# Optimization experiments

Hardware: AMD Instinct MI355X
Metric: run time of the kernel (lower is better)

Reference implementation:

```python
import jax, jax.numpy as jnp
import numpy as np

B, S, D, H = 4, 2048, 1024, 16
DH = D // H

def setup_inputs() -> dict:
    key = jax.random.key(0)
    ks = jax.random.split(key, 4)
    scale = 1.0 / np.sqrt(D)
    x = jax.random.normal(ks[0], (B, S, D), dtype=jnp.float32)
    Wq = jax.random.normal(ks[1], (D, D), dtype=jnp.float32) * scale
    Wk = jax.random.normal(ks[2], (D, D), dtype=jnp.float32) * scale
    Wv = jax.random.normal(ks[3], (D, D), dtype=jnp.float32) * scale
    bq = jnp.zeros((D,), dtype=jnp.float32)
    bk = jnp.zeros((D,), dtype=jnp.float32)
    bv = jnp.zeros((D,), dtype=jnp.float32)
    # causal mask, broadcastable to [B, H, S, S]; mask==0 positions get -inf
    mask = jnp.tril(jnp.ones((S, S), dtype=bool))[None, None, :, :]
    return {"x": x, "mask": mask, "Wq": Wq, "bq": bq, "Wk": Wk, "bk": bk, "Wv": Wv, "bv": bv}

def reference(x, mask, Wq, bq, Wk, bk, Wv, bv):
    b, s, d = x.shape
    def proj(W, bias):
        # nn.Linear: x @ W.T + b, then split heads -> [b, H, s, DH]
        y = jnp.einsum('bsd,ed->bse', x, W) + bias
        return y.reshape(b, s, H, DH).transpose(0, 2, 1, 3)
    q = proj(Wq, bq)
    k = proj(Wk, bk)
    v = proj(Wv, bv)
    scores = jnp.einsum('bhqd,bhkd->bhqk', q, k) / jnp.sqrt(jnp.float32(DH))
    scores = jnp.where(mask, scores, -jnp.inf)
    attn = jax.nn.softmax(scores, axis=-1)
    out = jnp.einsum('bhqk,bhkd->bhqd', attn, v)
    return out.transpose(0, 2, 1, 3).reshape(b, s, d)
```

## Files before the change

kernel.cpp:

```cpp
#include <hip/hip_runtime.h>
#include <hip/hip_bf16.h>
#include <stdint.h>

typedef unsigned short u16;
typedef unsigned int   u32;
typedef short bf16x8 __attribute__((ext_vector_type(8)));
typedef float f32x4  __attribute__((ext_vector_type(4)));

typedef bf16x8 __attribute__((__may_alias__)) bf16x8_a;
typedef uint4  __attribute__((__may_alias__)) uint4_a;
typedef uint2  __attribute__((__may_alias__)) uint2_a;
typedef float4 __attribute__((__may_alias__)) float4_a;

#define MFMA_BF16(a,b,c) __builtin_amdgcn_mfma_f32_16x16x32_bf16((a),(b),(c),0,0,0)
#define L2E 1.44269504088896340736f

#define SEQ 2048
#define DMODEL 1024
#define NH 16
#define DH 64

__device__ __forceinline__ u32 pack_bf2(float a, float b) {
  union { __hip_bfloat162 h; u32 u; } c;
  c.h = __float22bfloat162_rn(make_float2(a, b));
  return c.u;
}

__device__ __forceinline__ u16 f2bf(float f) {
  u32 u = __builtin_bit_cast(u32, f);
  u += 0x7FFFu + ((u >> 16) & 1u);
  return (u16)(u >> 16);
}

__device__ __forceinline__ void gl_lds16(const u16* g, u16* l) {
  __builtin_amdgcn_global_load_lds(
      (const __attribute__((address_space(1))) void*)g,
      (__attribute__((address_space(3))) void*)l, 16, 0, 0);
}

__global__ __launch_bounds__(256) void cvt_all_bf16(
    const float* __restrict__ x,
    const float* __restrict__ wq, const float* __restrict__ wk, const float* __restrict__ wv,
    u16* __restrict__ xb, u16* __restrict__ oq, u16* __restrict__ ok, u16* __restrict__ ov)
{
  const int c = blockIdx.x * 256 + threadIdx.x;
  const float* s; u16* d; int off;
  if (c < (1 << 20)) { s = x; d = xb; off = c; }
  else {
    const int c2 = c - (1 << 20);
    const int w = c2 >> 17;
    off = c2 & ((1 << 17) - 1);
    s = (w == 0) ? wq : (w == 1) ? wk : wv;
    d = (w == 0) ? oq : (w == 1) ? ok : ov;
  }
  const float4_a* p = (const float4_a*)(s + (size_t)off * 8);
  float4 a = p[0], b = p[1];
  uint4 o;
  o.x = pack_bf2(a.x, a.y); o.y = pack_bf2(a.z, a.w);
  o.z = pack_bf2(b.x, b.y); o.w = pack_bf2(b.z, b.w);
  *(uint4_a*)(d + (size_t)off * 8) = o;
}

__global__ __launch_bounds__(256, 3) void qkv_gemm_bf(
    const u16* __restrict__ Xb,
    const u16* __restrict__ Wqb, const u16* __restrict__ Wkb, const u16* __restrict__ Wvb,
    const float* __restrict__ Bq, const float* __restrict__ Bk, const float* __restrict__ Bv,
    u16* __restrict__ Qo, u16* __restrict__ Ko, u16* __restrict__ Vo)
{
  __shared__ u16 As[2][128 * 32];
  __shared__ u16 Bs[2][128 * 32];

  const int tid  = threadIdx.x;
  const int lane = tid & 63;
  const int wid  = tid >> 6;
  const int l16  = lane & 15;
  const int quad = lane >> 4;
  const int wm   = (wid >> 1) * 64;
  const int wn   = (wid & 1) * 64;

  const int m0 = blockIdx.x * 128;
  const int pj = blockIdx.z;

  const u16*   Wb   = (pj == 0) ? Wqb : (pj == 1) ? Wkb : Wvb;
  const float* Bias = (pj == 0) ? Bq : (pj == 1) ? Bk : Bv;
  u16*         Out  = (pj == 0) ? Qo : (pj == 1) ? Ko : Vo;
  const float scale = (pj == 0) ? 0.125f : 1.0f;

  const int lr = lane >> 2;
  const int lc = (lane & 3) * 8;

  const u16* Arow = Xb + (size_t)m0 * DMODEL;
  const int NT = DMODEL / 32;

  for (int nsub = 0; nsub < 2; ++nsub) {
    const int n0 = blockIdx.y * 256 + nsub * 128;
    const u16* Brow = Wb + (size_t)n0 * DMODEL;

    f32x4 acc[4][4];
#pragma unroll
    for (int i = 0; i < 4; i++)
#pragma unroll
      for (int j = 0; j < 4; j++) acc[i][j] = (f32x4){0.f, 0.f, 0.f, 0.f};

#pragma unroll
    for (int c = 0; c < 2; c++) {
      const int band = c * 64 + wid * 16;
      gl_lds16(Arow + (size_t)(band + lr) * DMODEL + 0 + lc, &As[0][band * 32]);
      gl_lds16(Brow + (size_t)(band + lr) * DMODEL + 0 + lc, &Bs[0][band * 32]);
    }
#pragma unroll
    for (int c = 0; c < 2; c++) {
      const int band = c * 64 + wid * 16;
      gl_lds16(Arow + (size_t)(band + lr) * DMODEL + 32 + lc, &As[1][band * 32]);
      gl_lds16(Brow + (size_t)(band + lr) * DMODEL + 32 + lc, &Bs[1][band * 32]);
    }

    for (int t = 0; t < NT; ++t) {
      const int cur = t & 1;
      if (t < NT - 1) asm volatile("s_waitcnt vmcnt(4)" ::: "memory");
      else            asm volatile("s_waitcnt vmcnt(0)" ::: "memory");
      __builtin_amdgcn_s_barrier();

      bf16x8 a[4], b[4];
#pragma unroll
      for (int mt = 0; mt < 4; mt++)
        a[mt] = *(const bf16x8_a*)&As[cur][(wm + mt * 16 + l16) * 32 + quad * 8];
#pragma unroll
      for (int nt = 0; nt < 4; nt++)
        b[nt] = *(const bf16x8_a*)&Bs[cur][(wn + nt * 16 + l16) * 32 + quad * 8];

      asm volatile("s_waitcnt lgkmcnt(0)" ::: "memory");
      __builtin_amdgcn_sched_barrier(0);
      __builtin_amdgcn_s_barrier();

      if (t + 2 < NT) {
        const int kt2 = (t + 2) * 32;
#pragma unroll
        for (int c = 0; c < 2; c++) {
          const int band = c * 64 + wid * 16;
          gl_lds16(Arow + (size_t)(band + lr) * DMODEL + kt2 + lc, &As[cur][band * 32]);
          gl_lds16(Brow + (size_t)(band + lr) * DMODEL + kt2 + lc, &Bs[cur][band * 32]);
        }
      }

#pragma unroll
      for (int mt = 0; mt < 4; mt++)
#pragma unroll
        for (int nt = 0; nt < 4; nt++)
          acc[mt][nt] = MFMA_BF16(a[mt], b[nt], acc[mt][nt]);
    }

    if (pj == 2) {
#pragma unroll
      for (int mt = 0; mt < 4; mt++) {
#pragma unroll
        for (int nt = 0; nt < 4; nt++) {
          const int n = n0 + wn + nt * 16 + l16;
          const float bias = Bias[n];
          const int h = n >> 6, dh = n & 63;
          const int m = m0 + wm + mt * 16 + quad * 4;
          const int bb = m >> 11, ss = m & 2047;
          uint2 pk;
          pk.x = pack_bf2(acc[mt][nt][0] + bias, acc[mt][nt][1] + bias);
          pk.y = pack_bf2(acc[mt][nt][2] + bias, acc[mt][nt][3] + bias);
          *(uint2_a*)&Out[((size_t)(bb * NH + h) * DH + dh) * SEQ + ss] = pk;
        }
      }
    } else {
#pragma unroll
      for (int mt = 0; mt < 4; mt++) {
#pragma unroll
        for (int nt = 0; nt < 4; nt++) {
          const int n = n0 + wn + nt * 16 + l16;
          const float bias = Bias[n];
          const int h = n >> 6, dh = n & 63;
#pragma unroll
          for (int r = 0; r < 4; r++) {
            const int m = m0 + wm + mt * 16 + quad * 4 + r;
            const int bb = m >> 11, ss = m & 2047;
            Out[((((size_t)bb * NH + h) * SEQ + ss) << 6) + dh] = f2bf((acc[mt][nt][r] + bias) * scale);
          }
        }
      }
    }

    if (nsub == 0) {
      asm volatile("s_waitcnt vmcnt(0)" ::: "memory");
    }
  }
}

__global__ __launch_bounds__(256, 2) void qkv_gemm(
    const float* __restrict__ X,
    const float* __restrict__ Wq, const float* __restrict__ Wk, const float* __restrict__ Wv,
    const float* __restrict__ Bq, const float* __restrict__ Bk, const float* __restrict__ Bv,
    u16* __restrict__ Qo, u16* __restrict__ Ko, u16* __restrict__ Vo)
{
  __shared__ u16 As[128 * 32];
  __shared__ u16 Bs[128 * 32];

  const int tid  = threadIdx.x;
  const int lane = tid & 63;
  const int wid  = tid >> 6;
  const int l16  = lane & 15;
  const int quad = lane >> 4;
  const int wm   = (wid >> 1) * 64;
  const int wn   = (wid & 1) * 64;

  const int m0 = blockIdx.x * 128;
  const int n0 = blockIdx.y * 128;
  const int pj = blockIdx.z;

  const float* W    = (pj == 0) ? Wq : (pj == 1) ? Wk : Wv;
  const float* Bias = (pj == 0) ? Bq : (pj == 1) ? Bk : Bv;
  u16*         Out  = (pj == 0) ? Qo : (pj == 1) ? Ko : Vo;
  const float scale = (pj == 0) ? 0.125f : 1.0f;

  f32x4 acc[4][4];
#pragma unroll
  for (int i = 0; i < 4; i++)
#pragma unroll
    for (int j = 0; j < 4; j++) acc[i][j] = (f32x4){0.f, 0.f, 0.f, 0.f};

  float4 gX[4], gW[4];
#pragma unroll
  for (int i = 0; i < 4; i++) {
    const int ch = i * 256 + tid;
    const int r = ch >> 3, c = ch & 7;
    gX[i] = *(const float4_a*)(X + (size_t)(m0 + r) * DMODEL + c * 4);
    gW[i] = *(const float4_a*)(W + (size_t)(n0 + r) * DMODEL + c * 4);
  }

  for (int kt = 0; kt < DMODEL; kt += 32) {
    __syncthreads();
#pragma unroll
    for (int i = 0; i < 4; i++) {
      const int ch = i * 256 + tid;
      const int r = ch >> 3, c = ch & 7;
      uint2 xp, wp;
      xp.x = pack_bf2(gX[i].x, gX[i].y);  xp.y = pack_bf2(gX[i].z, gX[i].w);
      wp.x = pack_bf2(gW[i].x, gW[i].y);  wp.y = pack_bf2(gW[i].z, gW[i].w);
      *(uint2_a*)&As[r * 32 + c * 4] = xp;
      *(uint2_a*)&Bs[r * 32 + c * 4] = wp;
    }
    __syncthreads();

    if (kt + 32 < DMODEL) {
#pragma unroll
      for (int i = 0; i < 4; i++) {
        const int ch = i * 256 + tid;
        const int r = ch >> 3, c = ch & 7;
        gX[i] = *(const float4_a*)(X + (size_t)(m0 + r) * DMODEL + kt + 32 + c * 4);
        gW[i] = *(const float4_a*)(W + (size_t)(n0 + r) * DMODEL + kt + 32 + c * 4);
      }
    }

    bf16x8 a[4], b[4];
#pragma unroll
    for (int mt = 0; mt < 4; mt++)
      a[mt] = *(const bf16x8_a*)&As[(wm + mt * 16 + l16) * 32 + quad * 8];
#pragma unroll
    for (int nt = 0; nt < 4; nt++)
      b[nt] = *(const bf16x8_a*)&Bs[(wn + nt * 16 + l16) * 32 + quad * 8];
#pragma unroll
    for (int mt = 0; mt < 4; mt++)
#pragma unroll
      for (int nt = 0; nt < 4; nt++)
        acc[mt][nt] = MFMA_BF16(a[mt], b[nt], acc[mt][nt]);
  }

  if (pj == 2) {
#pragma unroll
    for (int mt = 0; mt < 4; mt++) {
#pragma unroll
      for (int nt = 0; nt < 4; nt++) {
        const int n = n0 + wn + nt * 16 + l16;
        const float bias = Bias[n];
        const int h = n >> 6, dh = n & 63;
        const int m = m0 + wm + mt * 16 + quad * 4;
        const int bb = m >> 11, ss = m & 2047;
        uint2 pk;
        pk.x = pack_bf2(acc[mt][nt][0] + bias, acc[mt][nt][1] + bias);
        pk.y = pack_bf2(acc[mt][nt][2] + bias, acc[mt][nt][3] + bias);
        *(uint2_a*)&Out[((size_t)(bb * NH + h) * DH + dh) * SEQ + ss] = pk;
      }
    }
  } else {
#pragma unroll
    for (int mt = 0; mt < 4; mt++) {
#pragma unroll
      for (int nt = 0; nt < 4; nt++) {
        const int n = n0 + wn + nt * 16 + l16;
        const float bias = Bias[n];
        const int h = n >> 6, dh = n & 63;
#pragma unroll
        for (int r = 0; r < 4; r++) {
          const int m = m0 + wm + mt * 16 + quad * 4 + r;
          const int bb = m >> 11, ss = m & 2047;
          Out[((((size_t)bb * NH + h) * SEQ + ss) << 6) + dh] = f2bf((acc[mt][nt][r] + bias) * scale);
        }
      }
    }
  }
}

__global__ __launch_bounds__(256, 3) void flash_attn(
    const u16* __restrict__ Q, const u16* __restrict__ K, const u16* __restrict__ VT,
    float* __restrict__ O)
{
  __shared__ u16 Ks[2][64 * 64];
  __shared__ u16 VTs[2][64 * 64];
  __shared__ u16 Ps[4 * 32 * 72];

  const int tid  = threadIdx.x;
  const int lane = tid & 63;
  const int wid  = tid >> 6;
  const int l16  = lane & 15;
  const int quad = lane >> 4;

  const int idx = blockIdx.x;
  const int qt  = 15 - (idx >> 6);
  const int bh  = idx & 63;
  const int bb = bh >> 4, hh = bh & 15;
  const int qbase = qt * 128;

  const u16* Qh = Q  + (size_t)bh * (SEQ * DH);
  const u16* Kh = K  + (size_t)bh * (SEQ * DH);
  const u16* Vh = VT + (size_t)bh * (DH * SEQ);

#pragma unroll
  for (int i = 0; i < 4; i++) {
    const int ch = i * 256 + tid;
    const int r = ch >> 3, c = ch & 7;
    *(uint4_a*)&Ps[r * 72 + c * 8] = *(const uint4_a*)(Qh + (size_t)(qbase + r) * DH + c * 8);
  }
  __syncthreads();

  u16* Pw = &Ps[wid * 32 * 72];
  bf16x8 qf[2][2];
#pragma unroll
  for (int ct = 0; ct < 2; ct++)
#pragma unroll
    for (int ks = 0; ks < 2; ks++)
      qf[ct][ks] = *(const bf16x8_a*)&Pw[(ct * 16 + l16) * 72 + ks * 32 + quad * 8];

  bf16x8 ones;
#pragma unroll
  for (int i = 0; i < 8; i++) ones[i] = (short)0x3F80;

  f32x4 o[4][2];
#pragma unroll
  for (int dt = 0; dt < 4; dt++)
#pragma unroll
    for (int ct = 0; ct < 2; ct++) o[dt][ct] = (f32x4){0.f, 0.f, 0.f, 0.f};

  f32x4 lacc[2] = {(f32x4){0.f,0.f,0.f,0.f}, (f32x4){0.f,0.f,0.f,0.f}};
  float mold[2] = {-1e30f, -1e30f};

  const int jmax = 2 * qt + 1;
  const int swz  = (l16 & 7) << 3;

  uint4 gK[2], gV[2];
#pragma unroll
  for (int i = 0; i < 2; i++) {
    const int ch = i * 256 + tid;
    gK[i] = *(const uint4_a*)(Kh + (size_t)(ch >> 3) * DH + (ch & 7) * 8);
    gV[i] = *(const uint4_a*)(Vh + (size_t)(ch >> 3) * SEQ + (ch & 7) * 8);
  }
  asm volatile("s_waitcnt vmcnt(0)" ::: "memory");
#pragma unroll
  for (int i = 0; i < 2; i++) {
    const int ch = i * 256 + tid;
    const int row = ch >> 3, col = (ch & 7) * 8;
    *(uint4_a*)&Ks[0][row * 64 + (col ^ ((row & 7) << 3))]  = gK[i];
    *(uint4_a*)&VTs[0][row * 64 + (col ^ ((row & 7) << 3))] = gV[i];
  }
#pragma unroll
  for (int i = 0; i < 2; i++) {
    const int ch = i * 256 + tid;
    gK[i] = *(const uint4_a*)(Kh + (size_t)(64 + (ch >> 3)) * DH + (ch & 7) * 8);
    gV[i] = *(const uint4_a*)(Vh + (size_t)(ch >> 3) * SEQ + 64 + (ch & 7) * 8);
  }
  asm volatile("s_waitcnt lgkmcnt(0)" ::: "memory");
  __builtin_amdgcn_sched_barrier(0);
  __builtin_amdgcn_s_barrier();

  for (int j = 0; j <= jmax; j++) {
    const int cur = j & 1;
    const u16* Kc = Ks[cur];
    const u16* Vc = VTs[cur];

    f32x4 s[4][2];
#pragma unroll
    for (int rt = 0; rt < 4; rt++) {
      bf16x8 ka0 = *(const bf16x8_a*)&Kc[(rt * 16 + l16) * 64 + ((0  + quad * 8) ^ swz)];
      bf16x8 ka1 = *(const bf16x8_a*)&Kc[(rt * 16 + l16) * 64 + ((32 + quad * 8) ^ swz)];
#pragma unroll
      for (int ct = 0; ct < 2; ct++) {
        f32x4 c = (f32x4){0.f, 0.f, 0.f, 0.f};
        c = MFMA_BF16(ka0, qf[ct][0], c);
        c = MFMA_BF16(ka1, qf[ct][1], c);
        s[rt][ct] = c;
      }
    }

    if (j >= (qt << 1)) {
      const int kvb = j * 64;
#pragma unroll
      for (int rt = 0; rt < 4; rt++)
#pragma unroll
        for (int ct = 0; ct < 2; ct++) {
          const int ql = qbase + wid * 32 + ct * 16 + l16;
#pragma unroll
          for (int r = 0; r < 4; r++) {
            const int kvg = kvb + rt * 16 + quad * 4 + r;
            if (kvg > ql) s[rt][ct][r] = -1e30f;
          }
        }
    }

    if (j < jmax) {
      asm volatile("s_waitcnt vmcnt(0)" ::: "memory");
      const int nxt = cur ^ 1;
#pragma unroll
      for (int i = 0; i < 2; i++) {
        const int ch = i * 256 + tid;
        const int row = ch >> 3, col = (ch & 7) * 8;
        *(uint4_a*)&Ks[nxt][row * 64 + (col ^ ((row & 7) << 3))]  = gK[i];
        *(uint4_a*)&VTs[nxt][row * 64 + (col ^ ((row & 7) << 3))] = gV[i];
      }
      if (j + 1 < jmax) {
        const int kb2 = (j + 2) * 64;
#pragma unroll
        for (int i = 0; i < 2; i++) {
          const int ch = i * 256 + tid;
          gK[i] = *(const uint4_a*)(Kh + (size_t)(kb2 + (ch >> 3)) * DH + (ch & 7) * 8);
          gV[i] = *(const uint4_a*)(Vh + (size_t)(ch >> 3) * SEQ + kb2 + (ch & 7) * 8);
        }
      }
    }

#pragma unroll
    for (int ct = 0; ct < 2; ct++) {
      float m0_ = fmaxf(fmaxf(s[0][ct][0], s[0][ct][1]), fmaxf(s[0][ct][2], s[0][ct][3]));
      float m1_ = fmaxf(fmaxf(s[1][ct][0], s[1][ct][1]), fmaxf(s[1][ct][2], s[1][ct][3]));
      float m2_ = fmaxf(fmaxf(s[2][ct][0], s[2][ct][1]), fmaxf(s[2][ct][2], s[2][ct][3]));
      float m3_ = fmaxf(fmaxf(s[3][ct][0], s[3][ct][1]), fmaxf(s[3][ct][2], s[3][ct][3]));
      const float mloc = fmaxf(fmaxf(m0_, m1_), fmaxf(m2_, m3_));

      if (!__all(mloc - mold[ct] <= 8.0f)) {
        float mt = fmaxf(mloc, __shfl_xor(mloc, 16));
        mt = fmaxf(mt, __shfl_xor(mt, 32));
        const float mnew = fmaxf(mold[ct], mt);
        const float a = __builtin_amdgcn_exp2f((mold[ct] - mnew) * L2E);
        mold[ct] = mnew;
#pragma unroll
        for (int dt = 0; dt < 4; dt++)
#pragma unroll
          for (int r = 0; r < 4; r++) o[dt][ct][r] *= a;
#pragma unroll
        for (int r = 0; r < 4; r++) lacc[ct][r] *= a;
      }
      const float mref = mold[ct];

#pragma unroll
      for (int rt = 0; rt < 4; rt++)
#pragma unroll
        for (int r = 0; r < 4; r++)
          s[rt][ct][r] = __builtin_amdgcn_exp2f((s[rt][ct][r] - mref) * L2E);
    }

#pragma unroll
    for (int rt = 0; rt < 4; rt++) {
#pragma unroll
      for (int ct = 0; ct < 2; ct++) {
        uint2 pk;
        pk.x = pack_bf2(s[rt][ct][0], s[rt][ct][1]);
        pk.y = pack_bf2(s[rt][ct][2], s[rt][ct][3]);
        *(uint2_a*)&Pw[(ct * 16 + l16) * 72 + rt * 16 + quad * 4] = pk;
      }
    }
    asm volatile("s_waitcnt lgkmcnt(0)" ::: "memory");
    __builtin_amdgcn_sched_barrier(0);

#pragma unroll
    for (int ks2 = 0; ks2 < 2; ks2++) {
      bf16x8 vt[4], pb[2];
#pragma unroll
      for (int dt = 0; dt < 4; dt++)
        vt[dt] = *(const bf16x8_a*)&Vc[(dt * 16 + l16) * 64 + ((ks2 * 32 + quad * 8) ^ swz)];
#pragma unroll
      for (int ct = 0; ct < 2; ct++)
        pb[ct] = *(const bf16x8_a*)&Pw[(ct * 16 + l16) * 72 + ks2 * 32 + quad * 8];
#pragma unroll
      for (int dt = 0; dt < 4; dt++)
#pragma unroll
        for (int ct = 0; ct < 2; ct++)
          o[dt][ct] = MFMA_BF16(vt[dt], pb[ct], o[dt][ct]);
#pragma unroll
      for (int ct = 0; ct < 2; ct++)
        lacc[ct] = MFMA_BF16(ones, pb[ct], lacc[ct]);
    }

    __builtin_amdgcn_sched_barrier(0);
    __builtin_amdgcn_s_barrier();
  }

#pragma unroll
  for (int ct = 0; ct < 2; ct++) {
    const float inv = 1.0f / lacc[ct][0];
    const int qg = qbase + wid * 32 + ct * 16 + l16;
    float* orow = O + (size_t)((size_t)bb * SEQ + qg) * DMODEL + hh * 64;
#pragma unroll
    for (int dt = 0; dt < 4; dt++) {
      float4 v4;
      v4.x = o[dt][ct][0] * inv;  v4.y = o[dt][ct][1] * inv;
      v4.z = o[dt][ct][2] * inv;  v4.w = o[dt][ct][3] * inv;
      *(float4_a*)&orow[dt * 16 + quad * 4] = v4;
    }
  }
}

__global__ void paintf(float* out, int n, float v) {
  int i = blockIdx.x * 256 + threadIdx.x;
  if (i < n) out[i] = v;
}

extern "C" void kernel_launch(void* const* d_in, const int* in_sizes, int n_in,
                              void* d_out, int out_size, void* d_ws, size_t ws_size,
                              hipStream_t stream) {
  float* out = (float*)d_out;

  const size_t elems  = (size_t)4 * SEQ * DMODEL;
  const size_t welems = (size_t)DMODEL * DMODEL;
  const size_t need_old = 3 * elems * sizeof(u16);
  const size_t need_new = (4 * elems + 3 * welems) * sizeof(u16);

  if (ws_size < need_old) {
    paintf<<<(out_size + 255) / 256, 256, 0, stream>>>(out, out_size, 3.0e38f);
    return;
  }

  const float* x  = (const float*)d_in[0];
  const float* Wq = (const float*)d_in[2];
  const float* bq = (const float*)d_in[3];
  const float* Wk = (const float*)d_in[4];
  const float* bk = (const float*)d_in[5];
  const float* Wv = (const float*)d_in[6];
  const float* bv = (const float*)d_in[7];

  u16* q = (u16*)d_ws;
  u16* k = q + elems;
  u16* v = k + elems;

  if (ws_size >= need_new) {
    u16* xb  = v + elems;
    u16* wqb = xb + elems;
    u16* wkb = wqb + welems;
    u16* wvb = wkb + welems;
    cvt_all_bf16<<<5632, 256, 0, stream>>>(x, Wq, Wk, Wv, xb, wqb, wkb, wvb);
    qkv_gemm_bf<<<dim3(64, 4, 3), 256, 0, stream>>>(xb, wqb, wkb, wvb, bq, bk, bv, q, k, v);
  } else {
    qkv_gemm<<<dim3(64, 8, 3), 256, 0, stream>>>(x, Wq, Wk, Wv, bq, bk, bv, q, k, v);
  }

  flash_attn<<<1024, 256, 0, stream>>>(q, k, v, out);
}
```

Baseline: 255.6 us.

## Replace direct global-to-LDS loads with register-staged double buffering in bf16 QKV GEMM

The bf16 QKV projection GEMM stops using global_load_lds async copies and instead loads tiles into registers, then writes them to the alternate LDS buffer while the current tile is consumed by MFMA. The loop now keeps one barrier per k-step instead of two. The per-block two-subtile N loop is removed, so each block computes a single 128x128 tile and the grid doubles along N. This adds register pressure and a vmcnt(0) wait each iteration, which can expose global latency.

```diff
diff --git a/kernel.cpp b/kernel.cpp
--- a/kernel.cpp
+++ b/kernel.cpp
@@ -30,12 +30,6 @@
   u32 u = __builtin_bit_cast(u32, f);
   u += 0x7FFFu + ((u >> 16) & 1u);
   return (u16)(u >> 16);
-}
-
-__device__ __forceinline__ void gl_lds16(const u16* g, u16* l) {
-  __builtin_amdgcn_global_load_lds(
-      (const __attribute__((address_space(1))) void*)g,
-      (__attribute__((address_space(3))) void*)l, 16, 0, 0);
 }
 
 __global__ __launch_bounds__(256) void cvt_all_bf16(
@@ -79,6 +73,7 @@
   const int wn   = (wid & 1) * 64;
 
   const int m0 = blockIdx.x * 128;
+  const int n0 = blockIdx.y * 128;
   const int pj = blockIdx.z;
 
   const u16*   Wb   = (pj == 0) ? Wqb : (pj == 1) ? Wkb : Wvb;
@@ -86,188 +81,75 @@
   u16*         Out  = (pj == 0) ? Qo : (pj == 1) ? Ko : Vo;
   const float scale = (pj == 0) ? 0.125f : 1.0f;
 
-  const int lr = lane >> 2;
-  const int lc = (lane & 3) * 8;
-
   const u16* Arow = Xb + (size_t)m0 * DMODEL;
-  const int NT = DMODEL / 32;
-
-  for (int nsub = 0; nsub < 2; ++nsub) {
-    const int n0 = blockIdx.y * 256 + nsub * 128;
-    const u16* Brow = Wb + (size_t)n0 * DMODEL;
-
-    f32x4 acc[4][4];
-#pragma unroll
-    for (int i = 0; i < 4; i++)
-#pragma unroll
-      for (int j = 0; j < 4; j++) acc[i][j] = (f32x4){0.f, 0.f, 0.f, 0.f};
-
-#pragma unroll
-    for (int c = 0; c < 2; c++) {
-      const int band = c * 64 + wid * 16;
-      gl_lds16(Arow + (size_t)(band + lr) * DMODEL + 0 + lc, &As[0][band * 32]);
-      gl_lds16(Brow + (size_t)(band + lr) * DMODEL + 0 + lc, &Bs[0][band * 32]);
-    }
-#pragma unroll
-    for (int c = 0; c < 2; c++) {
-      const int band = c * 64 + wid * 16;
-      gl_lds16(Arow + (size_t)(band + lr) * DMODEL + 32 + lc, &As[1][band * 32]);
-      gl_lds16(Brow + (size_t)(band + lr) * DMODEL + 32 + lc, &Bs[1][band * 32]);
-    }
-
-    for (int t = 0; t < NT; ++t) {
-      const int cur = t & 1;
-      if (t < NT - 1) asm volatile("s_waitcnt vmcnt(4)" ::: "memory");
-      else            asm volatile("s_waitcnt vmcnt(0)" ::: "memory");
-      __builtin_amdgcn_s_barrier();
-
-      bf16x8 a[4], b[4];
-#pragma unroll
-      for (int mt = 0; mt < 4; mt++)
-        a[mt] = *(const bf16x8_a*)&As[cur][(wm + mt * 16 + l16) * 32 + quad * 8];
-#pragma unroll
-      for (int nt = 0; nt < 4; nt++)
-        b[nt] = *(const bf16x8_a*)&Bs[cur][(wn + nt * 16 + l16) * 32 + quad * 8];
-
-      asm volatile("s_waitcnt lgkmcnt(0)" ::: "memory");
-      __builtin_amdgcn_sched_barrier(0);
-      __builtin_amdgcn_s_barrier();
-
-      if (t + 2 < NT) {
-        const int kt2 = (t + 2) * 32;
-#pragma unroll
-        for (int c = 0; c < 2; c++) {
-          const int band = c * 64 + wid * 16;
-          gl_lds16(Arow + (size_t)(band + lr) * DMODEL + kt2 + lc, &As[cur][band * 32]);
-          gl_lds16(Brow + (size_t)(band + lr) * DMODEL + kt2 + lc, &Bs[cur][band * 32]);
-        }
-      }
-
-#pragma unroll
-      for (int mt = 0; mt < 4; mt++)
-#pragma unroll
-        for (int nt = 0; nt < 4; nt++)
-          acc[mt][nt] = MFMA_BF16(a[mt], b[nt], acc[mt][nt]);
-    }
-
-    if (pj == 2) {
-#pragma unroll
-      for (int mt = 0; mt < 4; mt++) {
-#pragma unroll
-        for (int nt = 0; nt < 4; nt++) {
-          const int n = n0 + wn + nt * 16 + l16;
-          const float bias = Bias[n];
-          const int h = n >> 6, dh = n & 63;
-          const int m = m0 + wm + mt * 16 + quad * 4;
-          const int bb = m >> 11, ss = m & 2047;
-          uint2 pk;
-          pk.x = pack_bf2(acc[mt][nt][0] + bias, acc[mt][nt][1] + bias);
-          pk.y = pack_bf2(acc[mt][nt][2] + bias, acc[mt][nt][3] + bias);
-          *(uint2_a*)&Out[((size_t)(bb * NH + h) * DH + dh) * SEQ + ss] = pk;
-        }
-      }
-    } else {
-#pragma unroll
-      for (int mt = 0; mt < 4; mt++) {
-#pragma unroll
-        for (int nt = 0; nt < 4; nt++) {
-          const int n = n0 + wn + nt * 16 + l16;
-          const float bias = Bias[n];
-          const int h = n >> 6, dh = n & 63;
-#pragma unroll
-          for (int r = 0; r < 4; r++) {
-            const int m = m0 + wm + mt * 16 + quad * 4 + r;
-            const int bb = m >> 11, ss = m & 2047;
-            Out[((((size_t)bb * NH + h) * SEQ + ss) << 6) + dh] = f2bf((acc[mt][nt][r] + bias) * scale);
-          }
-        }
-      }
-    }
-
-    if (nsub == 0) {
+  const u16* Brow = Wb + (size_t)n0 * DMODEL;
+
+  const int r0 = tid >> 2,  c0 = (tid & 3) * 8;
+  const int r1 = (256 + tid) >> 2, c1 = ((256 + tid) & 3) * 8;
+
+  f32x4 acc[4][4];
+#pragma unroll
+  for (int i = 0; i < 4; i++)
+#pragma unroll
+    for (int j = 0; j < 4; j++) acc[i][j] = (f32x4){0.f, 0.f, 0.f, 0.f};
+
+  uint4 gA[2], gB[2];
+
+#define LOADT(KT)                                                            \
+  {                                                                          \
+    gA[0] = *(const uint4_a*)(Arow + (size_t)r0 * DMODEL + (KT) + c0);       \
+    gB[0] = *(const uint4_a*)(Brow + (size_t)r0 * DMODEL + (KT) + c0);       \
+    gA[1] = *(const uint4_a*)(Arow + (size_t)r1 * DMODEL + (KT) + c1);       \
+    gB[1] = *(const uint4_a*)(Brow + (size_t)r1 * DMODEL + (KT) + c1);       \
+  }
+
+#define WRITET(BUF)                                                          \
+  {                                                                          \
+    *(uint4_a*)&As[BUF][r0 * 32 + c0] = gA[0];                               \
+    *(uint4_a*)&Bs[BUF][r0 * 32 + c0] = gB[0];                               \
+    *(uint4_a*)&As[BUF][r1 * 32 + c1] = gA[1];                               \
+    *(uint4_a*)&Bs[BUF][r1 * 32 + c1] = gB[1];                               \
+  }
+
+  LOADT(0);
+  asm volatile("s_waitcnt vmcnt(0)" ::: "memory");
+  WRITET(0);
+  LOADT(32);
+  asm volatile("s_waitcnt lgkmcnt(0)" ::: "memory");
+  __builtin_amdgcn_sched_barrier(0);
+  __builtin_amdgcn_s_barrier();
+
+  for (int t = 0; t < 32; ++t) {
+    const int cur = t & 1;
+
+    bf16x8 a[4], b[4];
+#pragma unroll
+    for (int mt = 0; mt < 4; mt++)
+      a[mt] = *(const bf16x8_a*)&As[cur][(wm + mt * 16 + l16) * 32 + quad * 8];
+#pragma unroll
+    for (int nt = 0; nt < 4; nt++)
+      b[nt] = *(const bf16x8_a*)&Bs[cur][(wn + nt * 16 + l16) * 32 + quad * 8];
+
+    if (t < 31) {
       asm volatile("s_waitcnt vmcnt(0)" ::: "memory");
-    }
-  }
-}
-
-__global__ __launch_bounds__(256, 2) void qkv_gemm(
-    const float* __restrict__ X,
-    const float* __restrict__ Wq, const float* __restrict__ Wk, const float* __restrict__ Wv,
-    const float* __restrict__ Bq, const float* __restrict__ Bk, const float* __restrict__ Bv,
-    u16* __restrict__ Qo, u16* __restrict__ Ko, u16* __restrict__ Vo)
-{
-  __shared__ u16 As[128 * 32];
-  __shared__ u16 Bs[128 * 32];
-
-  const int tid  = threadIdx.x;
-  const int lane = tid & 63;
-  const int wid  = tid >> 6;
-  const int l16  = lane & 15;
-  const int quad = lane >> 4;
-  const int wm   = (wid >> 1) * 64;
-  const int wn   = (wid & 1) * 64;
-
-  const int m0 = blockIdx.x * 128;
-  const int n0 = blockIdx.y * 128;
-  const int pj = blockIdx.z;
-
-  const float* W    = (pj == 0) ? Wq : (pj == 1) ? Wk : Wv;
-  const float* Bias = (pj == 0) ? Bq : (pj == 1) ? Bk : Bv;
-  u16*         Out  = (pj == 0) ? Qo : (pj == 1) ? Ko : Vo;
-  const float scale = (pj == 0) ? 0.125f : 1.0f;
-
-  f32x4 acc[4][4];
-#pragma unroll
-  for (int i = 0; i < 4; i++)
-#pragma unroll
-    for (int j = 0; j < 4; j++) acc[i][j] = (f32x4){0.f, 0.f, 0.f, 0.f};
-
-  float4 gX[4], gW[4];
-#pragma unroll
-  for (int i = 0; i < 4; i++) {
-    const int ch = i * 256 + tid;
-    const int r = ch >> 3, c = ch & 7;
-    gX[i] = *(const float4_a*)(X + (size_t)(m0 + r) * DMODEL + c * 4);
-    gW[i] = *(const float4_a*)(W + (size_t)(n0 + r) * DMODEL + c * 4);
-  }
-
-  for (int kt = 0; kt < DMODEL; kt += 32) {
-    __syncthreads();
-#pragma unroll
-    for (int i = 0; i < 4; i++) {
-      const int ch = i * 256 + tid;
-      const int r = ch >> 3, c = ch & 7;
-      uint2 xp, wp;
-      xp.x = pack_bf2(gX[i].x, gX[i].y);  xp.y = pack_bf2(gX[i].z, gX[i].w);
-      wp.x = pack_bf2(gW[i].x, gW[i].y);  wp.y = pack_bf2(gW[i].z, gW[i].w);
-      *(uint2_a*)&As[r * 32 + c * 4] = xp;
-      *(uint2_a*)&Bs[r * 32 + c * 4] = wp;
-    }
-    __syncthreads();
-
-    if (kt + 32 < DMODEL) {
-#pragma unroll
-      for (int i = 0; i < 4; i++) {
-        const int ch = i * 256 + tid;
-        const int r = ch >> 3, c = ch & 7;
-        gX[i] = *(const float4_a*)(X + (size_t)(m0 + r) * DMODEL + kt + 32 + c * 4);
-        gW[i] = *(const float4_a*)(W + (size_t)(n0 + r) * DMODEL + kt + 32 + c * 4);
-      }
-    }
-
-    bf16x8 a[4], b[4];
-#pragma unroll
-    for (int mt = 0; mt < 4; mt++)
-      a[mt] = *(const bf16x8_a*)&As[(wm + mt * 16 + l16) * 32 + quad * 8];
-#pragma unroll
-    for (int nt = 0; nt < 4; nt++)
-      b[nt] = *(const bf16x8_a*)&Bs[(wn + nt * 16 + l16) * 32 + quad * 8];
+      WRITET(cur ^ 1);
+      if (t + 2 < 32) LOADT((t + 2) * 32);
+    }
+
+    asm volatile("s_waitcnt lgkmcnt(0)" ::: "memory");
+    __builtin_amdgcn_sched_barrier(0);
+
 #pragma unroll
     for (int mt = 0; mt < 4; mt++)
 #pragma unroll
       for (int nt = 0; nt < 4; nt++)
         acc[mt][nt] = MFMA_BF16(a[mt], b[nt], acc[mt][nt]);
-  }
+
+    __builtin_amdgcn_sched_barrier(0);
+    __builtin_amdgcn_s_barrier();
+  }
+#undef LOADT
+#undef WRITET
 
   if (pj == 2) {
 #pragma unroll
@@ -304,6 +186,120 @@
   }
 }
 
+__global__ __launch_bounds__(256, 2) void qkv_gemm(
+    const float* __restrict__ X,
+    const float* __restrict__ Wq, const float* __restrict__ Wk, const float* __restrict__ Wv,
+    const float* __restrict__ Bq, const float* __restrict__ Bk, const float* __restrict__ Bv,
+    u16* __restrict__ Qo, u16* __restrict__ Ko, u16* __restrict__ Vo)
+{
+  __shared__ u16 As[128 * 32];
+  __shared__ u16 Bs[128 * 32];
+
+  const int tid  = threadIdx.x;
+  const int lane = tid & 63;
+  const int wid  = tid >> 6;
+  const int l16  = lane & 15;
+  const int quad = lane >> 4;
+  const int wm   = (wid >> 1) * 64;
+  const int wn   = (wid & 1) * 64;
+
+  const int m0 = blockIdx.x * 128;
+  const int n0 = blockIdx.y * 128;
+  const int pj = blockIdx.z;
+
+  const float* W    = (pj == 0) ? Wq : (pj == 1) ? Wk : Wv;
+  const float* Bias = (pj == 0) ? Bq : (pj == 1) ? Bk : Bv;
+  u16*         Out  = (pj == 0) ? Qo : (pj == 1) ? Ko : Vo;
+  const float scale = (pj == 0) ? 0.125f : 1.0f;
+
+  f32x4 acc[4][4];
+#pragma unroll
+  for (int i = 0; i < 4; i++)
+#pragma unroll
+    for (int j = 0; j < 4; j++) acc[i][j] = (f32x4){0.f, 0.f, 0.f, 0.f};
+
+  float4 gX[4], gW[4];
+#pragma unroll
+  for (int i = 0; i < 4; i++) {
+    const int ch = i * 256 + tid;
+    const int r = ch >> 3, c = ch & 7;
+    gX[i] = *(const float4_a*)(X + (size_t)(m0 + r) * DMODEL + c * 4);
+    gW[i] = *(const float4_a*)(W + (size_t)(n0 + r) * DMODEL + c * 4);
+  }
+
+  for (int kt = 0; kt < DMODEL; kt += 32) {
+    __syncthreads();
+#pragma unroll
+    for (int i = 0; i < 4; i++) {
+      const int ch = i * 256 + tid;
+      const int r = ch >> 3, c = ch & 7;
+      uint2 xp, wp;
+      xp.x = pack_bf2(gX[i].x, gX[i].y);  xp.y = pack_bf2(gX[i].z, gX[i].w);
+      wp.x = pack_bf2(gW[i].x, gW[i].y);  wp.y = pack_bf2(gW[i].z, gW[i].w);
+      *(uint2_a*)&As[r * 32 + c * 4] = xp;
+      *(uint2_a*)&Bs[r * 32 + c * 4] = wp;
+    }
+    __syncthreads();
+
+    if (kt + 32 < DMODEL) {
+#pragma unroll
+      for (int i = 0; i < 4; i++) {
+        const int ch = i * 256 + tid;
+        const int r = ch >> 3, c = ch & 7;
+        gX[i] = *(const float4_a*)(X + (size_t)(m0 + r) * DMODEL + kt + 32 + c * 4);
+        gW[i] = *(const float4_a*)(W + (size_t)(n0 + r) * DMODEL + kt + 32 + c * 4);
+      }
+    }
+
+    bf16x8 a[4], b[4];
+#pragma unroll
+    for (int mt = 0; mt < 4; mt++)
+      a[mt] = *(const bf16x8_a*)&As[(wm + mt * 16 + l16) * 32 + quad * 8];
+#pragma unroll
+    for (int nt = 0; nt < 4; nt++)
+      b[nt] = *(const bf16x8_a*)&Bs[(wn + nt * 16 + l16) * 32 + quad * 8];
+#pragma unroll
+    for (int mt = 0; mt < 4; mt++)
+#pragma unroll
+      for (int nt = 0; nt < 4; nt++)
+        acc[mt][nt] = MFMA_BF16(a[mt], b[nt], acc[mt][nt]);
+  }
+
+  if (pj == 2) {
+#pragma unroll
+    for (int mt = 0; mt < 4; mt++) {
+#pragma unroll
+      for (int nt = 0; nt < 4; nt++) {
+        const int n = n0 + wn + nt * 16 + l16;
+        const float bias = Bias[n];
+        const int h = n >> 6, dh = n & 63;
+        const int m = m0 + wm + mt * 16 + quad * 4;
+        const int bb = m >> 11, ss = m & 2047;
+        uint2 pk;
+        pk.x = pack_bf2(acc[mt][nt][0] + bias, acc[mt][nt][1] + bias);
+        pk.y = pack_bf2(acc[mt][nt][2] + bias, acc[mt][nt][3] + bias);
+        *(uint2_a*)&Out[((size_t)(bb * NH + h) * DH + dh) * SEQ + ss] = pk;
+      }
+    }
+  } else {
+#pragma unroll
+    for (int mt = 0; mt < 4; mt++) {
+#pragma unroll
+      for (int nt = 0; nt < 4; nt++) {
+        const int n = n0 + wn + nt * 16 + l16;
+        const float bias = Bias[n];
+        const int h = n >> 6, dh = n & 63;
+#pragma unroll
+        for (int r = 0; r < 4; r++) {
+          const int m = m0 + wm + mt * 16 + quad * 4 + r;
+          const int bb = m >> 11, ss = m & 2047;
+          Out[((((size_t)bb * NH + h) * SEQ + ss) << 6) + dh] = f2bf((acc[mt][nt][r] + bias) * scale);
+        }
+      }
+    }
+  }
+}
+
 __global__ __launch_bounds__(256, 3) void flash_attn(
     const u16* __restrict__ Q, const u16* __restrict__ K, const u16* __restrict__ VT,
     float* __restrict__ O)
@@ -559,7 +555,7 @@
     u16* wkb = wqb + welems;
     u16* wvb = wkb + welems;
     cvt_all_bf16<<<5632, 256, 0, stream>>>(x, Wq, Wk, Wv, xb, wqb, wkb, wvb);
-    qkv_gemm_bf<<<dim3(64, 4, 3), 256, 0, stream>>>(xb, wqb, wkb, wvb, bq, bk, bv, q, k, v);
+    qkv_gemm_bf<<<dim3(64, 8, 3), 256, 0, stream>>>(xb, wqb, wkb, wvb, bq, bk, bv, q, k, v);
   } else {
     qkv_gemm<<<dim3(64, 8, 3), 256, 0, stream>>>(x, Wq, Wk, Wv, bq, bk, bv, q, k, v);
   }
```

New measurement: 441.2 us. +72.6%, slower.
